# Kernel tuning notes

Measured on AMD Instinct MI355X. Metric: run time of the kernel, lower is better.

Reference implementation:

```python
import jax, jax.numpy as jnp
import numpy as np

B, LQ, LK = 8, 1024, 1024
Q_IN, K_IN, D = 256, 256, 512
H = 8
DK = D // H


def _linear_params(key, in_dim, out_dim):
    k1, k2 = jax.random.split(key)
    bound = 1.0 / np.sqrt(in_dim)
    W = jax.random.uniform(k1, (in_dim, out_dim), jnp.float32, -bound, bound)
    b = jax.random.uniform(k2, (out_dim,), jnp.float32, -bound, bound)
    return W, b


def setup_inputs() -> dict:
    key = jax.random.key(0)
    ks = jax.random.split(key, 7)
    query = jax.random.normal(ks[0], (B, LQ, Q_IN), jnp.float32)
    kv = jax.random.normal(ks[1], (B, LK, K_IN), jnp.float32)
    mask = jax.random.randint(ks[2], (B, LQ, LK), 0, 2, jnp.int32)
    Wq, bq = _linear_params(ks[3], Q_IN, D)
    Wk, bk = _linear_params(ks[4], K_IN, D)
    Wv, bv = _linear_params(ks[5], K_IN, D)
    Wo, bo = _linear_params(ks[6], D, D)
    return {"query": query, "key": kv, "mask": mask,
            "Wq": Wq, "bq": bq, "Wk": Wk, "bk": bk,
            "Wv": Wv, "bv": bv, "Wo": Wo, "bo": bo}


def reference(query, key, mask, Wq, bq, Wk, bk, Wv, bv, Wo, bo):
    b = query.shape[0]
    # ReLU-activated QKV projections
    q = jax.nn.relu(query @ Wq + bq)   # [B, Lq, D]
    v = jax.nn.relu(key @ Wv + bv)     # [B, Lk, D]
    k = jax.nn.relu(key @ Wk + bk)     # [B, Lk, D]
    # split heads: [B, H, L, d_k]
    q = q.reshape(b, -1, H, DK).transpose(0, 2, 1, 3)
    k = k.reshape(b, -1, H, DK).transpose(0, 2, 1, 3)
    v = v.reshape(b, -1, H, DK).transpose(0, 2, 1, 3)
    scores = jnp.einsum('bhqd,bhkd->bhqk', q, k) / jnp.sqrt(jnp.float32(DK))
    scores = jnp.where(mask[:, None, :, :] == 0, jnp.float32(-1e8), scores)
    attn = jax.nn.softmax(scores, axis=-1)
    out = jnp.einsum('bhqk,bhkd->bhqd', attn, v)
    out = out.transpose(0, 2, 1, 3).reshape(b, -1, D)
    return out @ Wo + bo
```

## Files before the change

### kernel.cpp

```cpp
#include <hip/hip_runtime.h>
#include <hip/hip_bf16.h>
#include <type_traits>

typedef __bf16 bf16_t;
typedef __bf16 bf16x4 __attribute__((ext_vector_type(4)));
typedef __bf16 bf16x8 __attribute__((ext_vector_type(8)));
typedef float  f32x4  __attribute__((ext_vector_type(4)));

__device__ __forceinline__ f32x4 mfma16(bf16x8 a, bf16x8 b, f32x4 c) {
  return __builtin_amdgcn_mfma_f32_16x16x32_bf16(a, b, c, 0, 0, 0);
}

static constexpr int NB = 8;
static constexpr int LQ = 1024;
static constexpr int LKk = 1024;
static constexpr int DMODEL = 512;
static constexpr int NH = 8;
static constexpr int DKH = 64;
static constexpr int MROWS = NB * LQ;
static constexpr int MWORDS = NB * LQ * (LKk / 64);
#define KSCALE 0.1803368801111204f

__device__ __forceinline__ int swz(int row, int byte) {
  return row * 128 + (byte ^ ((row & 7) << 4));
}

__global__ __launch_bounds__(256)
void mask_pack(const int* __restrict__ mask, unsigned long long* __restrict__ mpk) {
  const int wd = blockIdx.x * 256 + threadIdx.x;
  const int4* base = reinterpret_cast<const int4*>(mask + (size_t)wd * 64);
  unsigned long long bits = 0;
  #pragma unroll
  for (int i = 0; i < 16; ++i) {
    int4 v = base[i];
    bits |= (unsigned long long)(v.x != 0) << (4 * i);
    bits |= (unsigned long long)(v.y != 0) << (4 * i + 1);
    bits |= (unsigned long long)(v.z != 0) << (4 * i + 2);
    bits |= (unsigned long long)(v.w != 0) << (4 * i + 3);
  }
  mpk[wd] = bits;
}

__device__ __forceinline__ void wt_tile(const float* __restrict__ W, bf16_t* __restrict__ Wt,
                                        int K, int N, int kt, int nt, int t) {
  __shared__ bf16_t T[64][72];
  const int k0 = kt * 64, n0 = nt * 64;
  const int kr = t >> 2, c0 = (t & 3) * 16;
  const float4* src = reinterpret_cast<const float4*>(W + (size_t)(k0 + kr) * N + n0 + c0);
  #pragma unroll
  for (int j = 0; j < 4; ++j) {
    float4 f = src[j];
    T[c0 + j * 4 + 0][kr] = (bf16_t)f.x;
    T[c0 + j * 4 + 1][kr] = (bf16_t)f.y;
    T[c0 + j * 4 + 2][kr] = (bf16_t)f.z;
    T[c0 + j * 4 + 3][kr] = (bf16_t)f.w;
  }
  __syncthreads();
  const int nr = t >> 2, kc0 = (t & 3) * 16;
  bf16_t* dst = Wt + (size_t)(n0 + nr) * K + k0 + kc0;
  #pragma unroll
  for (int j = 0; j < 2; ++j)
    *reinterpret_cast<bf16x8*>(dst + j * 8) =
        *reinterpret_cast<const bf16x8*>(&T[nr][kc0 + j * 8]);
}

__global__ __launch_bounds__(256)
void weight_prep(const float* __restrict__ Wq, const float* __restrict__ Wk,
                 const float* __restrict__ Wv, const float* __restrict__ Wo,
                 bf16_t* __restrict__ Wtq, bf16_t* __restrict__ Wtk,
                 bf16_t* __restrict__ Wtv, bf16_t* __restrict__ Wto) {
  const int bidx = blockIdx.x, t = threadIdx.x;
  if (bidx < 32)        wt_tile(Wq, Wtq, 256, 512, bidx >> 3, bidx & 7, t);
  else if (bidx < 64)   wt_tile(Wk, Wtk, 256, 512, (bidx - 32) >> 3, bidx & 7, t);
  else if (bidx < 96)   wt_tile(Wv, Wtv, 256, 512, (bidx - 64) >> 3, bidx & 7, t);
  else                  wt_tile(Wo, Wto, 512, 512, (bidx - 96) >> 3, bidx & 7, t);
}

template<int K, bool RELU, typename AT, typename OT>
__global__ __launch_bounds__(256)
void gemm_bias_act(const AT* __restrict__ A, const bf16_t* __restrict__ Wt,
                   const float* __restrict__ bias, OT* __restrict__ C,
                   float postscale)
{
  constexpr int N = 512;
  __shared__ alignas(16) char Alds[64 * 128];
  __shared__ alignas(16) char Wlds[64 * 128];
  const int t = threadIdx.x;
  const int l = t & 63, w = t >> 6;
  const int xcd = blockIdx.x & 7, idx = blockIdx.x >> 3;
  const int m0 = (xcd * 16 + (idx >> 3)) * 64, n0 = (idx & 7) * 64;

  f32x4 acc[4] = {};
  for (int k0 = 0; k0 < K; k0 += 64) {
    __syncthreads();
    if constexpr (std::is_same<AT, float>::value) {
      const int row = t >> 2, c0 = (t & 3) * 16;
      const float4* ap = reinterpret_cast<const float4*>(A + (size_t)(m0 + row) * K + k0 + c0);
      #pragma unroll
      for (int j = 0; j < 4; ++j) {
        float4 f = ap[j];
        bf16x4 o = { (bf16_t)f.x, (bf16_t)f.y, (bf16_t)f.z, (bf16_t)f.w };
        *reinterpret_cast<bf16x4*>(&Alds[swz(row, (c0 + j * 4) * 2)]) = o;
      }
    } else {
      const int row = t >> 2, cb = ((2 * t) & 7) * 16;
      const bf16_t* src = A + (size_t)(m0 + row) * K + k0 + cb / 2;
      *reinterpret_cast<bf16x8*>(&Alds[swz(row, cb)]) = *reinterpret_cast<const bf16x8*>(src);
      *reinterpret_cast<bf16x8*>(&Alds[swz(row, cb + 16)]) = *reinterpret_cast<const bf16x8*>(src + 8);
    }
    {
      const int row = t >> 2, cb = ((2 * t) & 7) * 16;
      const bf16_t* src = Wt + (size_t)(n0 + row) * K + k0 + cb / 2;
      *reinterpret_cast<bf16x8*>(&Wlds[swz(row, cb)]) = *reinterpret_cast<const bf16x8*>(src);
      *reinterpret_cast<bf16x8*>(&Wlds[swz(row, cb + 16)]) = *reinterpret_cast<const bf16x8*>(src + 8);
    }
    __syncthreads();
    #pragma unroll
    for (int ks = 0; ks < 2; ++ks) {
      const int kb = (ks * 32 + ((l >> 4) * 8)) * 2;
      const int arow = w * 16 + (l & 15);
      bf16x8 af = *reinterpret_cast<const bf16x8*>(&Alds[swz(arow, kb)]);
      #pragma unroll
      for (int ct = 0; ct < 4; ++ct) {
        const int brow = ct * 16 + (l & 15);
        bf16x8 bfr = *reinterpret_cast<const bf16x8*>(&Wlds[swz(brow, kb)]);
        acc[ct] = mfma16(af, bfr, acc[ct]);
      }
    }
  }
  #pragma unroll
  for (int ct = 0; ct < 4; ++ct) {
    const int col = n0 + ct * 16 + (l & 15);
    const float bv = bias[col];
    #pragma unroll
    for (int r = 0; r < 4; ++r) {
      const int row = m0 + w * 16 + ((l >> 4) * 4) + r;
      float x = acc[ct][r] + bv;
      if constexpr (RELU) x = fmaxf(x, 0.f);
      C[(size_t)row * N + col] = (OT)(x * postscale);
    }
  }
}

__global__ __launch_bounds__(256)
void attn_kernel(const bf16_t* __restrict__ Qp, const bf16_t* __restrict__ Kp,
                 const bf16_t* __restrict__ Vp, const unsigned long long* __restrict__ Mpk,
                 bf16_t* __restrict__ AO)
{
  __shared__ alignas(16) char Klds[64 * 128];
  __shared__ alignas(16) char Vlds[64 * 128];
  __shared__ alignas(16) char Plds[4 * 32 * 128];
  const int t = threadIdx.x, l = t & 63, w = t >> 6;
  const int g = l >> 4, qh = l & 15;
  const int bid = (blockIdx.x & 7) * 64 + (blockIdx.x >> 3);
  const int qt = bid & 7, h = (bid >> 3) & 7, b = bid >> 6;
  const int wq0 = qt * 128 + w * 32;
  const size_t rb = (size_t)b * LQ;

  bf16x8 qf[2][2];
  #pragma unroll
  for (int j = 0; j < 2; ++j)
    #pragma unroll
    for (int ks = 0; ks < 2; ++ks)
      qf[j][ks] = *reinterpret_cast<const bf16x8*>(
          Qp + (rb + wq0 + j * 16 + qh) * DMODEL + h * DKH + ks * 32 + g * 8);

  const unsigned long long* mrow0 = Mpk + (rb + wq0 + qh) * (LKk / 64);
  const unsigned long long* mrow1 = Mpk + (rb + wq0 + 16 + qh) * (LKk / 64);

  f32x4 acc[2][4] = {};
  float mrun[2] = { -1e30f, -1e30f }, lsum[2] = { 0.f, 0.f };

  for (int kv0 = 0; kv0 < LKk; kv0 += 64) {
    const unsigned long long mw[2] = { mrow0[kv0 >> 6], mrow1[kv0 >> 6] };

    __syncthreads();
    {
      const int row = t >> 2, cb = ((2 * t) & 7) * 16;
      const bf16_t* src = Kp + (rb + kv0 + row) * DMODEL + h * DKH + cb / 2;
      *reinterpret_cast<bf16x8*>(&Klds[swz(row, cb)]) = *reinterpret_cast<const bf16x8*>(src);
      *reinterpret_cast<bf16x8*>(&Klds[swz(row, cb + 16)]) = *reinterpret_cast<const bf16x8*>(src + 8);
    }
    {
      const int kv = t & 63, d0 = (t >> 6) * 16;
      const bf16_t* s0 = Vp + (rb + kv0 + kv) * DMODEL + h * DKH + d0;
      bf16x8 v0 = *reinterpret_cast<const bf16x8*>(s0);
      bf16x8 v1 = *reinterpret_cast<const bf16x8*>(s0 + 8);
      #pragma unroll
      for (int i = 0; i < 8; ++i)
        *reinterpret_cast<bf16_t*>(&Vlds[swz(d0 + i, kv * 2)]) = v0[i];
      #pragma unroll
      for (int i = 0; i < 8; ++i)
        *reinterpret_cast<bf16_t*>(&Vlds[swz(d0 + 8 + i, kv * 2)]) = v1[i];
    }
    __syncthreads();

    f32x4 s[2][4] = {};
    #pragma unroll
    for (int ks = 0; ks < 2; ++ks) {
      const int kb = (ks * 32 + g * 8) * 2;
      #pragma unroll
      for (int ct = 0; ct < 4; ++ct) {
        bf16x8 kf = *reinterpret_cast<const bf16x8*>(&Klds[swz(ct * 16 + qh, kb)]);
        s[0][ct] = mfma16(kf, qf[0][ks], s[0][ct]);
        s[1][ct] = mfma16(kf, qf[1][ks], s[1][ct]);
      }
    }

    #pragma unroll
    for (int j = 0; j < 2; ++j) {
      float rmax = -1e30f;
      #pragma unroll
      for (int ct = 0; ct < 4; ++ct) {
        #pragma unroll
        for (int r = 0; r < 4; ++r) {
          float x = ((mw[j] >> (ct * 16 + g * 4 + r)) & 1) ? s[j][ct][r] : -1e8f;
          s[j][ct][r] = x;
          rmax = fmaxf(rmax, x);
        }
      }
      rmax = fmaxf(rmax, __shfl_xor(rmax, 16));
      rmax = fmaxf(rmax, __shfl_xor(rmax, 32));
      const float newm = fmaxf(mrun[j], rmax);

      if (__any(newm > mrun[j])) {
        const float scale = __builtin_amdgcn_exp2f(mrun[j] - newm);
        lsum[j] *= scale;
        #pragma unroll
        for (int r = 0; r < 4; ++r) {
          const float sr = __shfl(scale, g * 4 + r, 64);
          #pragma unroll
          for (int dct = 0; dct < 4; ++dct) acc[j][dct][r] *= sr;
        }
        mrun[j] = newm;
      }

      float psum = 0.f;
      #pragma unroll
      for (int ct = 0; ct < 4; ++ct) {
        #pragma unroll
        for (int r = 0; r < 4; ++r) {
          const float pv = __builtin_amdgcn_exp2f(s[j][ct][r] - mrun[j]);
          s[j][ct][r] = pv;
          psum += pv;
        }
      }
      psum += __shfl_xor(psum, 16);
      psum += __shfl_xor(psum, 32);
      lsum[j] += psum;

      #pragma unroll
      for (int ct = 0; ct < 4; ++ct) {
        #pragma unroll
        for (int r = 0; r < 4; ++r)
          *reinterpret_cast<bf16_t*>(
              &Plds[w * 4096 + swz(j * 16 + qh, (ct * 16 + g * 4 + r) * 2)]) =
              (bf16_t)s[j][ct][r];
      }
    }

    #pragma unroll
    for (int ks = 0; ks < 2; ++ks) {
      const int kb = (ks * 32 + g * 8) * 2;
      bf16x8 pf0 = *reinterpret_cast<const bf16x8*>(&Plds[w * 4096 + swz(qh, kb)]);
      bf16x8 pf1 = *reinterpret_cast<const bf16x8*>(&Plds[w * 4096 + swz(16 + qh, kb)]);
      #pragma unroll
      for (int dct = 0; dct < 4; ++dct) {
        bf16x8 vf = *reinterpret_cast<const bf16x8*>(&Vlds[swz(dct * 16 + qh, kb)]);
        acc[0][dct] = mfma16(pf0, vf, acc[0][dct]);
        acc[1][dct] = mfma16(pf1, vf, acc[1][dct]);
      }
    }
  }

  #pragma unroll
  for (int j = 0; j < 2; ++j) {
    const float inv = 1.0f / lsum[j];
    float invr[4];
    #pragma unroll
    for (int r = 0; r < 4; ++r) invr[r] = __shfl(inv, g * 4 + r, 64);
    #pragma unroll
    for (int dct = 0; dct < 4; ++dct) {
      const int col = h * DKH + dct * 16 + qh;
      #pragma unroll
      for (int r = 0; r < 4; ++r) {
        const int q = wq0 + j * 16 + g * 4 + r;
        AO[(rb + q) * DMODEL + col] = (bf16_t)(acc[j][dct][r] * invr[r]);
      }
    }
  }
}

extern "C" void kernel_launch(void* const* d_in, const int* in_sizes, int n_in,
                              void* d_out, int out_size, void* d_ws, size_t ws_size,
                              hipStream_t stream)
{
  const float* query = (const float*)d_in[0];
  const float* keyin = (const float*)d_in[1];
  const int*   mask  = (const int*)d_in[2];
  const float* Wq = (const float*)d_in[3];
  const float* bq = (const float*)d_in[4];
  const float* Wk = (const float*)d_in[5];
  const float* bk = (const float*)d_in[6];
  const float* Wv = (const float*)d_in[7];
  const float* bv = (const float*)d_in[8];
  const float* Wo = (const float*)d_in[9];
  const float* bo = (const float*)d_in[10];
  float* out = (float*)d_out;

  bf16_t* Qp = (bf16_t*)d_ws;
  bf16_t* Kp = Qp + (size_t)MROWS * DMODEL;
  bf16_t* Vp = Kp + (size_t)MROWS * DMODEL;
  bf16_t* AO = Vp + (size_t)MROWS * DMODEL;
  unsigned long long* Mpk = (unsigned long long*)(AO + (size_t)MROWS * DMODEL);
  bf16_t* Wtq = (bf16_t*)(Mpk + MWORDS);
  bf16_t* Wtk = Wtq + 512 * 256;
  bf16_t* Wtv = Wtk + 512 * 256;
  bf16_t* Wto = Wtv + 512 * 256;

  dim3 blk(256);

  weight_prep<<<dim3(160), blk, 0, stream>>>(Wq, Wk, Wv, Wo, Wtq, Wtk, Wtv, Wto);
  mask_pack<<<dim3(MWORDS / 256), blk, 0, stream>>>(mask, Mpk);
  gemm_bias_act<256, true,  float,  bf16_t><<<dim3(1024), blk, 0, stream>>>(query, Wtq, bq, Qp, 1.0f);
  gemm_bias_act<256, true,  float,  bf16_t><<<dim3(1024), blk, 0, stream>>>(keyin, Wtk, bk, Kp, KSCALE);
  gemm_bias_act<256, true,  float,  bf16_t><<<dim3(1024), blk, 0, stream>>>(keyin, Wtv, bv, Vp, 1.0f);

  attn_kernel<<<dim3(NB * NH * (LQ / 128)), blk, 0, stream>>>(Qp, Kp, Vp, Mpk, AO);

  gemm_bias_act<512, false, bf16_t, float><<<dim3(1024), blk, 0, stream>>>(AO, Wto, bo, out, 1.0f);
}
```

Measured before the change: 106.9 us.

## Fuse K/V projections and split attention KV range across two wave groups

New measurement: 106.1 us. About the same (-0.7%).

```diff
diff --git a/kernel.cpp b/kernel.cpp
--- a/kernel.cpp
+++ b/kernel.cpp
@@ -143,19 +143,91 @@
 }
 
 __global__ __launch_bounds__(256)
+void gemm_kv(const float* __restrict__ A, const bf16_t* __restrict__ Wtk,
+             const bf16_t* __restrict__ Wtv, const float* __restrict__ bk,
+             const float* __restrict__ bv, bf16_t* __restrict__ Ck,
+             bf16_t* __restrict__ Cv)
+{
+  constexpr int K = 256, N = 512;
+  __shared__ alignas(16) char Alds[64 * 128];
+  __shared__ alignas(16) char Wk_lds[64 * 128];
+  __shared__ alignas(16) char Wv_lds[64 * 128];
+  const int t = threadIdx.x;
+  const int l = t & 63, w = t >> 6;
+  const int xcd = blockIdx.x & 7, idx = blockIdx.x >> 3;
+  const int m0 = (xcd * 16 + (idx >> 3)) * 64, n0 = (idx & 7) * 64;
+
+  f32x4 acck[4] = {}, accv[4] = {};
+  for (int k0 = 0; k0 < K; k0 += 64) {
+    __syncthreads();
+    {
+      const int row = t >> 2, c0 = (t & 3) * 16;
+      const float4* ap = reinterpret_cast<const float4*>(A + (size_t)(m0 + row) * K + k0 + c0);
+      #pragma unroll
+      for (int j = 0; j < 4; ++j) {
+        float4 f = ap[j];
+        bf16x4 o = { (bf16_t)f.x, (bf16_t)f.y, (bf16_t)f.z, (bf16_t)f.w };
+        *reinterpret_cast<bf16x4*>(&Alds[swz(row, (c0 + j * 4) * 2)]) = o;
+      }
+    }
+    {
+      const int row = t >> 2, cb = ((2 * t) & 7) * 16;
+      const bf16_t* sk = Wtk + (size_t)(n0 + row) * K + k0 + cb / 2;
+      const bf16_t* sv = Wtv + (size_t)(n0 + row) * K + k0 + cb / 2;
+      *reinterpret_cast<bf16x8*>(&Wk_lds[swz(row, cb)]) = *reinterpret_cast<const bf16x8*>(sk);
+      *reinterpret_cast<bf16x8*>(&Wk_lds[swz(row, cb + 16)]) = *reinterpret_cast<const bf16x8*>(sk + 8);
+      *reinterpret_cast<bf16x8*>(&Wv_lds[swz(row, cb)]) = *reinterpret_cast<const bf16x8*>(sv);
+      *reinterpret_cast<bf16x8*>(&Wv_lds[swz(row, cb + 16)]) = *reinterpret_cast<const bf16x8*>(sv + 8);
+    }
+    __syncthreads();
+    #pragma unroll
+    for (int ks = 0; ks < 2; ++ks) {
+      const int kb = (ks * 32 + ((l >> 4) * 8)) * 2;
+      const int arow = w * 16 + (l & 15);
+      bf16x8 af = *reinterpret_cast<const bf16x8*>(&Alds[swz(arow, kb)]);
+      #pragma unroll
+      for (int ct = 0; ct < 4; ++ct) {
+        const int brow = ct * 16 + (l & 15);
+        bf16x8 bk8 = *reinterpret_cast<const bf16x8*>(&Wk_lds[swz(brow, kb)]);
+        bf16x8 bv8 = *reinterpret_cast<const bf16x8*>(&Wv_lds[swz(brow, kb)]);
+        acck[ct] = mfma16(af, bk8, acck[ct]);
+        accv[ct] = mfma16(af, bv8, accv[ct]);
+      }
+    }
+  }
+  #pragma unroll
+  for (int ct = 0; ct < 4; ++ct) {
+    const int col = n0 + ct * 16 + (l & 15);
+    const float bkv = bk[col], bvv = bv[col];
+    #pragma unroll
+    for (int r = 0; r < 4; ++r) {
+      const int row = m0 + w * 16 + ((l >> 4) * 4) + r;
+      Ck[(size_t)row * N + col] = (bf16_t)(fmaxf(acck[ct][r] + bkv, 0.f) * KSCALE);
+      Cv[(size_t)row * N + col] = (bf16_t)fmaxf(accv[ct][r] + bvv, 0.f);
+    }
+  }
+}
+
+__global__ __launch_bounds__(512)
 void attn_kernel(const bf16_t* __restrict__ Qp, const bf16_t* __restrict__ Kp,
                  const bf16_t* __restrict__ Vp, const unsigned long long* __restrict__ Mpk,
                  bf16_t* __restrict__ AO)
 {
-  __shared__ alignas(16) char Klds[64 * 128];
-  __shared__ alignas(16) char Vlds[64 * 128];
-  __shared__ alignas(16) char Plds[4 * 32 * 128];
-  const int t = threadIdx.x, l = t & 63, w = t >> 6;
+  __shared__ alignas(16) char SMEM[65536];
+  const int t = threadIdx.x, l = t & 63;
+  const int wave = t >> 6;
+  const int hw = wave >> 2;
+  const int w4 = wave & 3;
+  const int th = t & 255;
   const int g = l >> 4, qh = l & 15;
   const int bid = (blockIdx.x & 7) * 64 + (blockIdx.x >> 3);
   const int qt = bid & 7, h = (bid >> 3) & 7, b = bid >> 6;
-  const int wq0 = qt * 128 + w * 32;
+  const int wq0 = qt * 128 + w4 * 32;
   const size_t rb = (size_t)b * LQ;
+
+  char* Klds = SMEM + hw * 8192;
+  char* Vlds = SMEM + 16384 + hw * 8192;
+  char* Pw   = SMEM + 32768 + wave * 4096;
 
   bf16x8 qf[2][2];
   #pragma unroll
@@ -171,18 +243,20 @@
   f32x4 acc[2][4] = {};
   float mrun[2] = { -1e30f, -1e30f }, lsum[2] = { 0.f, 0.f };
 
-  for (int kv0 = 0; kv0 < LKk; kv0 += 64) {
+  const int kvbase = hw * 512;
+  for (int kt = 0; kt < 8; ++kt) {
+    const int kv0 = kvbase + kt * 64;
     const unsigned long long mw[2] = { mrow0[kv0 >> 6], mrow1[kv0 >> 6] };
 
     __syncthreads();
     {
-      const int row = t >> 2, cb = ((2 * t) & 7) * 16;
+      const int row = th >> 2, cb = ((2 * th) & 7) * 16;
       const bf16_t* src = Kp + (rb + kv0 + row) * DMODEL + h * DKH + cb / 2;
       *reinterpret_cast<bf16x8*>(&Klds[swz(row, cb)]) = *reinterpret_cast<const bf16x8*>(src);
       *reinterpret_cast<bf16x8*>(&Klds[swz(row, cb + 16)]) = *reinterpret_cast<const bf16x8*>(src + 8);
     }
     {
-      const int kv = t & 63, d0 = (t >> 6) * 16;
+      const int kv = th & 63, d0 = (th >> 6) * 16;
       const bf16_t* s0 = Vp + (rb + kv0 + kv) * DMODEL + h * DKH + d0;
       bf16x8 v0 = *reinterpret_cast<const bf16x8*>(s0);
       bf16x8 v1 = *reinterpret_cast<const bf16x8*>(s0 + 8);
@@ -254,16 +328,15 @@
         #pragma unroll
         for (int r = 0; r < 4; ++r)
           *reinterpret_cast<bf16_t*>(
-              &Plds[w * 4096 + swz(j * 16 + qh, (ct * 16 + g * 4 + r) * 2)]) =
-              (bf16_t)s[j][ct][r];
+              &Pw[swz(j * 16 + qh, (ct * 16 + g * 4 + r) * 2)]) = (bf16_t)s[j][ct][r];
       }
     }
 
     #pragma unroll
     for (int ks = 0; ks < 2; ++ks) {
       const int kb = (ks * 32 + g * 8) * 2;
-      bf16x8 pf0 = *reinterpret_cast<const bf16x8*>(&Plds[w * 4096 + swz(qh, kb)]);
-      bf16x8 pf1 = *reinterpret_cast<const bf16x8*>(&Plds[w * 4096 + swz(16 + qh, kb)]);
+      bf16x8 pf0 = *reinterpret_cast<const bf16x8*>(&Pw[swz(qh, kb)]);
+      bf16x8 pf1 = *reinterpret_cast<const bf16x8*>(&Pw[swz(16 + qh, kb)]);
       #pragma unroll
       for (int dct = 0; dct < 4; ++dct) {
         bf16x8 vf = *reinterpret_cast<const bf16x8*>(&Vlds[swz(dct * 16 + qh, kb)]);
@@ -273,19 +346,48 @@
     }
   }
 
-  #pragma unroll
-  for (int j = 0; j < 2; ++j) {
-    const float inv = 1.0f / lsum[j];
-    float invr[4];
-    #pragma unroll
-    for (int r = 0; r < 4; ++r) invr[r] = __shfl(inv, g * 4 + r, 64);
-    #pragma unroll
-    for (int dct = 0; dct < 4; ++dct) {
-      const int col = h * DKH + dct * 16 + qh;
+  __syncthreads();
+  float* creg = reinterpret_cast<float*>(SMEM + w4 * 9216);
+  if (hw == 1) {
+    creg[0 * 64 + l] = mrun[0];
+    creg[1 * 64 + l] = mrun[1];
+    creg[2 * 64 + l] = lsum[0];
+    creg[3 * 64 + l] = lsum[1];
+    #pragma unroll
+    for (int j = 0; j < 2; ++j)
+      #pragma unroll
+      for (int dct = 0; dct < 4; ++dct)
+        #pragma unroll
+        for (int r = 0; r < 4; ++r)
+          creg[(4 + j * 16 + dct * 4 + r) * 64 + l] = acc[j][dct][r];
+  }
+  __syncthreads();
+  if (hw == 0) {
+    #pragma unroll
+    for (int j = 0; j < 2; ++j) {
+      const float mb = creg[j * 64 + l];
+      const float lb = creg[(2 + j) * 64 + l];
+      const float m = fmaxf(mrun[j], mb);
+      const float wa = __builtin_amdgcn_exp2f(mrun[j] - m);
+      const float wb = __builtin_amdgcn_exp2f(mb - m);
+      const float inv = 1.0f / (lsum[j] * wa + lb * wb);
+      float war[4], wbr[4], invr[4];
       #pragma unroll
       for (int r = 0; r < 4; ++r) {
-        const int q = wq0 + j * 16 + g * 4 + r;
-        AO[(rb + q) * DMODEL + col] = (bf16_t)(acc[j][dct][r] * invr[r]);
+        war[r]  = __shfl(wa, g * 4 + r, 64);
+        wbr[r]  = __shfl(wb, g * 4 + r, 64);
+        invr[r] = __shfl(inv, g * 4 + r, 64);
+      }
+      #pragma unroll
+      for (int dct = 0; dct < 4; ++dct) {
+        const int col = h * DKH + dct * 16 + qh;
+        #pragma unroll
+        for (int r = 0; r < 4; ++r) {
+          const float ob = creg[(4 + j * 16 + dct * 4 + r) * 64 + l];
+          const int q = wq0 + j * 16 + g * 4 + r;
+          AO[(rb + q) * DMODEL + col] =
+              (bf16_t)((acc[j][dct][r] * war[r] + ob * wbr[r]) * invr[r]);
+        }
       }
     }
   }
@@ -322,11 +424,10 @@
 
   weight_prep<<<dim3(160), blk, 0, stream>>>(Wq, Wk, Wv, Wo, Wtq, Wtk, Wtv, Wto);
   mask_pack<<<dim3(MWORDS / 256), blk, 0, stream>>>(mask, Mpk);
-  gemm_bias_act<256, true,  float,  bf16_t><<<dim3(1024), blk, 0, stream>>>(query, Wtq, bq, Qp, 1.0f);
-  gemm_bias_act<256, true,  float,  bf16_t><<<dim3(1024), blk, 0, stream>>>(keyin, Wtk, bk, Kp, KSCALE);
-  gemm_bias_act<256, true,  float,  bf16_t><<<dim3(1024), blk, 0, stream>>>(keyin, Wtv, bv, Vp, 1.0f);
-
-  attn_kernel<<<dim3(NB * NH * (LQ / 128)), blk, 0, stream>>>(Qp, Kp, Vp, Mpk, AO);
+  gemm_bias_act<256, true, float, bf16_t><<<dim3(1024), blk, 0, stream>>>(query, Wtq, bq, Qp, 1.0f);
+  gemm_kv<<<dim3(1024), blk, 0, stream>>>(keyin, Wtk, Wtv, bk, bv, Kp, Vp);
+
+  attn_kernel<<<dim3(NB * NH * (LQ / 128)), dim3(512), 0, stream>>>(Qp, Kp, Vp, Mpk, AO);
 
   gemm_bias_act<512, false, bf16_t, float><<<dim3(1024), blk, 0, stream>>>(AO, Wto, bo, out, 1.0f);
 }
```

## Fuse K and V projections and emit V pre-transposed for attention

Applied to the files above, without the earlier changes.

Measured after the change: 97.43 us. -8.9%, faster.

```diff
diff --git a/kernel.cpp b/kernel.cpp
--- a/kernel.cpp
+++ b/kernel.cpp
@@ -143,8 +143,79 @@
 }
 
 __global__ __launch_bounds__(256)
+void gemm_kv(const float* __restrict__ A, const bf16_t* __restrict__ Wtk,
+             const bf16_t* __restrict__ Wtv, const float* __restrict__ bk,
+             const float* __restrict__ bv, bf16_t* __restrict__ Ck,
+             bf16_t* __restrict__ Vt)
+{
+  constexpr int K = 256, N = 512;
+  __shared__ alignas(16) char Alds[64 * 128];
+  __shared__ alignas(16) char Wk_lds[64 * 128];
+  __shared__ alignas(16) char Wv_lds[64 * 128];
+  const int t = threadIdx.x;
+  const int l = t & 63, w = t >> 6;
+  const int xcd = blockIdx.x & 7, idx = blockIdx.x >> 3;
+  const int m0 = (xcd * 16 + (idx >> 3)) * 64, n0 = (idx & 7) * 64;
+
+  f32x4 acck[4] = {}, accv[4] = {};
+  for (int k0 = 0; k0 < K; k0 += 64) {
+    __syncthreads();
+    {
+      const int row = t >> 2, c0 = (t & 3) * 16;
+      const float4* ap = reinterpret_cast<const float4*>(A + (size_t)(m0 + row) * K + k0 + c0);
+      #pragma unroll
+      for (int j = 0; j < 4; ++j) {
+        float4 f = ap[j];
+        bf16x4 o = { (bf16_t)f.x, (bf16_t)f.y, (bf16_t)f.z, (bf16_t)f.w };
+        *reinterpret_cast<bf16x4*>(&Alds[swz(row, (c0 + j * 4) * 2)]) = o;
+      }
+    }
+    {
+      const int row = t >> 2, cb = ((2 * t) & 7) * 16;
+      const bf16_t* sk = Wtk + (size_t)(n0 + row) * K + k0 + cb / 2;
+      const bf16_t* sv = Wtv + (size_t)(n0 + row) * K + k0 + cb / 2;
+      *reinterpret_cast<bf16x8*>(&Wk_lds[swz(row, cb)]) = *reinterpret_cast<const bf16x8*>(sk);
+      *reinterpret_cast<bf16x8*>(&Wk_lds[swz(row, cb + 16)]) = *reinterpret_cast<const bf16x8*>(sk + 8);
+      *reinterpret_cast<bf16x8*>(&Wv_lds[swz(row, cb)]) = *reinterpret_cast<const bf16x8*>(sv);
+      *reinterpret_cast<bf16x8*>(&Wv_lds[swz(row, cb + 16)]) = *reinterpret_cast<const bf16x8*>(sv + 8);
+    }
+    __syncthreads();
+    #pragma unroll
+    for (int ks = 0; ks < 2; ++ks) {
+      const int kb = (ks * 32 + ((l >> 4) * 8)) * 2;
+      const int arow = w * 16 + (l & 15);
+      bf16x8 af = *reinterpret_cast<const bf16x8*>(&Alds[swz(arow, kb)]);
+      #pragma unroll
+      for (int ct = 0; ct < 4; ++ct) {
+        const int brow = ct * 16 + (l & 15);
+        bf16x8 bk8 = *reinterpret_cast<const bf16x8*>(&Wk_lds[swz(brow, kb)]);
+        bf16x8 bv8 = *reinterpret_cast<const bf16x8*>(&Wv_lds[swz(brow, kb)]);
+        acck[ct] = mfma16(af, bk8, acck[ct]);
+        accv[ct] = mfma16(af, bv8, accv[ct]);
+      }
+    }
+  }
+  const int row0 = m0 + w * 16 + ((l >> 4) * 4);
+  const int vb = row0 >> 10;
+  const int kv = row0 & 1023;
+  #pragma unroll
+  for (int ct = 0; ct < 4; ++ct) {
+    const int col = n0 + ct * 16 + (l & 15);
+    const float bkv = bk[col], bvv = bv[col];
+    #pragma unroll
+    for (int r = 0; r < 4; ++r)
+      Ck[(size_t)(row0 + r) * N + col] = (bf16_t)(fmaxf(acck[ct][r] + bkv, 0.f) * KSCALE);
+    bf16x4 vv;
+    #pragma unroll
+    for (int r = 0; r < 4; ++r) vv[r] = (bf16_t)fmaxf(accv[ct][r] + bvv, 0.f);
+    bf16_t* dst = Vt + (((size_t)vb * NH + (col >> 6)) * DKH + (col & 63)) * LKk + kv;
+    *reinterpret_cast<bf16x4*>(dst) = vv;
+  }
+}
+
+__global__ __launch_bounds__(256)
 void attn_kernel(const bf16_t* __restrict__ Qp, const bf16_t* __restrict__ Kp,
-                 const bf16_t* __restrict__ Vp, const unsigned long long* __restrict__ Mpk,
+                 const bf16_t* __restrict__ Vt, const unsigned long long* __restrict__ Mpk,
                  bf16_t* __restrict__ AO)
 {
   __shared__ alignas(16) char Klds[64 * 128];
@@ -156,6 +227,7 @@
   const int qt = bid & 7, h = (bid >> 3) & 7, b = bid >> 6;
   const int wq0 = qt * 128 + w * 32;
   const size_t rb = (size_t)b * LQ;
+  const bf16_t* vtb = Vt + ((size_t)b * NH + h) * DKH * LKk;
 
   bf16x8 qf[2][2];
   #pragma unroll
@@ -182,16 +254,10 @@
       *reinterpret_cast<bf16x8*>(&Klds[swz(row, cb + 16)]) = *reinterpret_cast<const bf16x8*>(src + 8);
     }
     {
-      const int kv = t & 63, d0 = (t >> 6) * 16;
-      const bf16_t* s0 = Vp + (rb + kv0 + kv) * DMODEL + h * DKH + d0;
-      bf16x8 v0 = *reinterpret_cast<const bf16x8*>(s0);
-      bf16x8 v1 = *reinterpret_cast<const bf16x8*>(s0 + 8);
-      #pragma unroll
-      for (int i = 0; i < 8; ++i)
-        *reinterpret_cast<bf16_t*>(&Vlds[swz(d0 + i, kv * 2)]) = v0[i];
-      #pragma unroll
-      for (int i = 0; i < 8; ++i)
-        *reinterpret_cast<bf16_t*>(&Vlds[swz(d0 + 8 + i, kv * 2)]) = v1[i];
+      const int row = t >> 2, cb = ((2 * t) & 7) * 16;
+      const bf16_t* src = vtb + (size_t)row * LKk + kv0 + cb / 2;
+      *reinterpret_cast<bf16x8*>(&Vlds[swz(row, cb)]) = *reinterpret_cast<const bf16x8*>(src);
+      *reinterpret_cast<bf16x8*>(&Vlds[swz(row, cb + 16)]) = *reinterpret_cast<const bf16x8*>(src + 8);
     }
     __syncthreads();
 
@@ -310,8 +376,8 @@
 
   bf16_t* Qp = (bf16_t*)d_ws;
   bf16_t* Kp = Qp + (size_t)MROWS * DMODEL;
-  bf16_t* Vp = Kp + (size_t)MROWS * DMODEL;
-  bf16_t* AO = Vp + (size_t)MROWS * DMODEL;
+  bf16_t* Vt = Kp + (size_t)MROWS * DMODEL;
+  bf16_t* AO = Vt + (size_t)MROWS * DMODEL;
   unsigned long long* Mpk = (unsigned long long*)(AO + (size_t)MROWS * DMODEL);
   bf16_t* Wtq = (bf16_t*)(Mpk + MWORDS);
   bf16_t* Wtk = Wtq + 512 * 256;
@@ -322,11 +388,10 @@
 
   weight_prep<<<dim3(160), blk, 0, stream>>>(Wq, Wk, Wv, Wo, Wtq, Wtk, Wtv, Wto);
   mask_pack<<<dim3(MWORDS / 256), blk, 0, stream>>>(mask, Mpk);
-  gemm_bias_act<256, true,  float,  bf16_t><<<dim3(1024), blk, 0, stream>>>(query, Wtq, bq, Qp, 1.0f);
-  gemm_bias_act<256, true,  float,  bf16_t><<<dim3(1024), blk, 0, stream>>>(keyin, Wtk, bk, Kp, KSCALE);
-  gemm_bias_act<256, true,  float,  bf16_t><<<dim3(1024), blk, 0, stream>>>(keyin, Wtv, bv, Vp, 1.0f);
-
-  attn_kernel<<<dim3(NB * NH * (LQ / 128)), blk, 0, stream>>>(Qp, Kp, Vp, Mpk, AO);
+  gemm_bias_act<256, true, float, bf16_t><<<dim3(1024), blk, 0, stream>>>(query, Wtq, bq, Qp, 1.0f);
+  gemm_kv<<<dim3(1024), blk, 0, stream>>>(keyin, Wtk, Wtv, bk, bv, Kp, Vt);
+
+  attn_kernel<<<dim3(NB * NH * (LQ / 128)), blk, 0, stream>>>(Qp, Kp, Vt, Mpk, AO);
 
   gemm_bias_act<512, false, bf16_t, float><<<dim3(1024), blk, 0, stream>>>(AO, Wto, bo, out, 1.0f);
 }
```
